# Performance work log

Hardware: AMD Instinct MI355X
Metric: run time of the kernel (lower is better)

The kernel has to match this reference:

```python
import jax, jax.numpy as jnp
import numpy as np

B, S, F, DK = 8, 2048, 1024, 128

def setup_inputs() -> dict:
    key = jax.random.key(0)
    ks = jax.random.split(key, 6)
    scale = 0.02
    return {
        "q": jax.random.normal(ks[0], (B, S, F), dtype=jnp.float32),
        "k": jax.random.normal(ks[1], (B, S, F), dtype=jnp.float32),
        "v": jax.random.normal(ks[2], (B, S, F), dtype=jnp.float32),
        "w_q": jax.random.normal(ks[3], (F, DK), dtype=jnp.float32) * scale,
        "w_k": jax.random.normal(ks[4], (F, DK), dtype=jnp.float32) * scale,
        "w_v": jax.random.normal(ks[5], (F, DK), dtype=jnp.float32) * scale,
    }

def reference(q, k, v, w_q, w_k, w_v):
    d_k = w_q.shape[-1]
    # bias-free linear projections: [B,S,F] @ [F,DK] -> [B,S,DK]
    qp = jnp.einsum("bsf,fd->bsd", q, w_q)
    kp = jnp.einsum("bsf,fd->bsd", k, w_k)
    vp = jnp.einsum("bsf,fd->bsd", v, w_v)
    # scaled dot-product scores: [B,S,S]
    scores = jnp.einsum("bqd,bkd->bqk", qp, kp) * (1.0 / jnp.sqrt(jnp.float32(d_k)))
    attn = jax.nn.softmax(scores, axis=-1)
    out = jnp.einsum("bqk,bkd->bqd", attn, vp)
    return out
```

## Files before the change

### kernel.cpp

```cpp
#include <hip/hip_runtime.h>
#include <hip/hip_bf16.h>

#define B_ 8
#define S_ 2048
#define F_ 1024
#define DK_ 128
#define M_ (B_*S_)

typedef unsigned short u16;
typedef short short8 __attribute__((ext_vector_type(8)));
typedef float f32x4 __attribute__((ext_vector_type(4)));
typedef float f32x16 __attribute__((ext_vector_type(16)));

__device__ __forceinline__ u16 f2bf(float f) {
    unsigned int u = __float_as_uint(f);
    u += 0x7FFFu + ((u >> 16) & 1u);
    return (u16)(u >> 16);
}
__device__ __forceinline__ unsigned int pack2(float a, float b) {
    return (unsigned int)f2bf(a) | ((unsigned int)f2bf(b) << 16);
}
__device__ __forceinline__ float fexp2(float x) {
#if __has_builtin(__builtin_amdgcn_exp2f)
    return __builtin_amdgcn_exp2f(x);
#else
    return exp2f(x);
#endif
}
__device__ __forceinline__ unsigned int cvt_pk_bf16(float lo, float hi) {
    unsigned int r;
    asm("v_cvt_pk_bf16_f32 %0, %1, %2" : "=v"(r) : "v"(lo), "v"(hi));
    return r;
}
__device__ __forceinline__ void pl32_swap(unsigned int& a, unsigned int& b) {
    asm("v_permlane32_swap_b32 %0, %1" : "+v"(a), "+v"(b));
}

__global__ __launch_bounds__(256) void prep_wt(const float* __restrict__ wq,
                                               const float* __restrict__ wk,
                                               const float* __restrict__ wv,
                                               u16* __restrict__ WT) {
    int id = blockIdx.x * 256 + threadIdx.x;
    if (id >= 3 * DK_ * F_) return;
    int m   = id / (DK_ * F_);
    int rem = id - m * (DK_ * F_);
    int c   = rem / F_;
    int k   = rem - c * F_;
    const float* w = (m == 0) ? wq : (m == 1) ? wk : wv;
    float v = w[k * DK_ + c];
    if (m == 0) v *= 0.12751741951f;
    WT[id] = f2bf(v);
}

__global__ __launch_bounds__(256, 3) void proj(const float* __restrict__ xq,
                                               const float* __restrict__ xk,
                                               const float* __restrict__ xv,
                                               const u16* __restrict__ WT,
                                               u16* __restrict__ qfr,
                                               u16* __restrict__ kfr,
                                               u16* __restrict__ vfr) {
    const int mode = blockIdx.y;
    const float* X = (mode == 0) ? xq : (mode == 1) ? xk : xv;
    const u16*   W = WT + mode * (DK_ * F_);

    __shared__ u16 a_lds[64][40];
    __shared__ u16 w_lds[128][40];

    const int t    = threadIdx.x;
    const int lane = t & 63;
    const int wv_  = t >> 6;
    const int l15  = lane & 15, l4 = lane >> 4;
    const int row0 = blockIdx.x * 64;

    f32x4 acc[8];
#pragma unroll
    for (int j = 0; j < 8; ++j) acc[j] = f32x4{0.f, 0.f, 0.f, 0.f};

    for (int k0 = 0; k0 < F_; k0 += 32) {
        {
            int r = t >> 2, kk = (t & 3) * 8;
            const float4* src = (const float4*)(X + (size_t)(row0 + r) * F_ + k0 + kk);
            float4 f0 = src[0], f1 = src[1];
            int4 o0;
            o0.x = pack2(f0.x, f0.y); o0.y = pack2(f0.z, f0.w);
            o0.z = pack2(f1.x, f1.y); o0.w = pack2(f1.z, f1.w);
            *(int4*)&a_lds[r][kk] = o0;
        }
        {
            int c = t >> 1, kk = (t & 1) * 16;
            const int4* src = (const int4*)(W + (size_t)c * F_ + k0 + kk);
            *(int4*)&w_lds[c][kk]     = src[0];
            *(int4*)&w_lds[c][kk + 8] = src[1];
        }
        __syncthreads();

        short8 af = *(const short8*)&a_lds[wv_ * 16 + l15][l4 * 8];
        short8 bf[8];
#pragma unroll
        for (int ct = 0; ct < 8; ++ct)
            bf[ct] = *(const short8*)&w_lds[ct * 16 + l15][l4 * 8];

        if (mode < 2) {
#pragma unroll
            for (int ct = 0; ct < 8; ++ct)
                acc[ct] = __builtin_amdgcn_mfma_f32_16x16x32_bf16(af, bf[ct], acc[ct], 0, 0, 0);
        } else {
#pragma unroll
            for (int ct = 0; ct < 8; ++ct)
                acc[ct] = __builtin_amdgcn_mfma_f32_16x16x32_bf16(bf[ct], af, acc[ct], 0, 0, 0);
        }
        __syncthreads();
    }

    if (mode < 2) {
        u16* OUT = (mode == 0) ? qfr : kfr;
#pragma unroll
        for (int ct = 0; ct < 8; ++ct)
#pragma unroll
            for (int r = 0; r < 4; ++r) {
                int q = row0 + wv_ * 16 + l4 * 4 + r;
                int d = ct * 16 + l15;
                int g = q >> 5, j = q & 31;
                int c = d >> 4, h2 = (d >> 3) & 1, e = d & 7;
                OUT[(((size_t)g * 8 + c) * 64 + h2 * 32 + j) * 8 + e] = f2bf(acc[ct][r]);
            }
    } else {
#pragma unroll
        for (int ct = 0; ct < 8; ++ct)
#pragma unroll
            for (int r = 0; r < 4; ++r) {
                int d = ct * 16 + l4 * 4 + r;
                int m = row0 + wv_ * 16 + l15;
                int g = m >> 5, ch = (m >> 4) & 1, h2 = (m >> 3) & 1, e = m & 7;
                int ct2 = d >> 5, l31 = d & 31;
                vfr[((((size_t)g * 4 + ct2) * 2 + ch) * 64 + h2 * 32 + l31) * 8 + e]
                    = f2bf(acc[ct][r]);
            }
    }
}

__global__ __launch_bounds__(512)
__attribute__((amdgpu_waves_per_eu(2)))
void attn(const u16* __restrict__ qfr,
          const u16* __restrict__ kfr,
          const u16* __restrict__ vfr,
          float* __restrict__ out) {
    __shared__ float ob[64][132];
    __shared__ float m_l[2][4][32], l_l[2][4][2][32], gm_l[2][32], gl_l[2][32];

    const int t      = threadIdx.x;
    const int lane   = t & 63;
    const int wv_    = t >> 6;
    const int q_sub  = wv_ & 1;
    const int kv_sub = wv_ >> 1;
    const int r31    = lane & 31;
    const int hi     = lane >> 5;

    const int b  = blockIdx.x & 7;
    const int qi = blockIdx.x >> 3;
    const int qrow0 = b * S_ + qi * 64;

    const size_t qg = (size_t)(b * 64 + qi * 2 + q_sub);
    short8 qf[8];
#pragma unroll
    for (int c = 0; c < 8; ++c)
        qf[c] = *(const short8*)(qfr + (qg * 8 + c) * 512 + lane * 8);

    f32x16 o4[4];
#pragma unroll
    for (int ct = 0; ct < 4; ++ct)
#pragma unroll
        for (int i = 0; i < 16; ++i) o4[ct][i] = 0.f;
    float mrun = -1.0e30f, lrun = 0.f;

    short8 kf[8];
    {
        const size_t g0 = (size_t)(b * 64 + kv_sub);
#pragma unroll
        for (int c = 0; c < 8; ++c)
            kf[c] = *(const short8*)(kfr + (g0 * 8 + c) * 512 + lane * 8);
    }

    for (int kt = 0; kt < 16; ++kt) {
        const size_t g = (size_t)(b * 64 + kt * 4 + kv_sub);

        f32x16 sa, sb;
#pragma unroll
        for (int i = 0; i < 16; ++i) { sa[i] = 0.f; sb[i] = 0.f; }
#pragma unroll
        for (int c = 0; c < 4; ++c) {
            sa = __builtin_amdgcn_mfma_f32_32x32x16_bf16(kf[c],     qf[c],     sa, 0, 0, 0);
            sb = __builtin_amdgcn_mfma_f32_32x32x16_bf16(kf[c + 4], qf[c + 4], sb, 0, 0, 0);
        }
        f32x16 st;
#pragma unroll
        for (int i = 0; i < 16; ++i) st[i] = sa[i] + sb[i];

        short8 vf[4][2];
#pragma unroll
        for (int ct = 0; ct < 4; ++ct)
#pragma unroll
            for (int ch = 0; ch < 2; ++ch)
                vf[ct][ch] = *(const short8*)(vfr + (((g * 4 + ct) * 2 + ch) * 64 + lane) * 8);

        float tm = st[0];
#pragma unroll
        for (int i = 1; i < 16; ++i) tm = fmaxf(tm, st[i]);
        if (__any(tm > mrun + 8.0f)) {
            tm = fmaxf(tm, __shfl_xor(tm, 32, 64));
            float mn = fmaxf(mrun, tm);
            float fs = fexp2(mrun - mn);
            mrun = mn;
            lrun *= fs;
#pragma unroll
            for (int ct = 0; ct < 4; ++ct)
#pragma unroll
                for (int i = 0; i < 16; ++i) o4[ct][i] *= fs;
        }
        float s0 = 0.f, s1 = 0.f;
#pragma unroll
        for (int i = 0; i < 16; i += 2) {
            st[i]     = fexp2(st[i] - mrun);
            st[i + 1] = fexp2(st[i + 1] - mrun);
            s0 += st[i]; s1 += st[i + 1];
        }
        lrun += s0 + s1;

        short8 bp[2];
#pragma unroll
        for (int ch = 0; ch < 2; ++ch) {
            unsigned int A1 = cvt_pk_bf16(st[ch * 8 + 0], st[ch * 8 + 1]);
            unsigned int A2 = cvt_pk_bf16(st[ch * 8 + 2], st[ch * 8 + 3]);
            unsigned int A3 = cvt_pk_bf16(st[ch * 8 + 4], st[ch * 8 + 5]);
            unsigned int A4 = cvt_pk_bf16(st[ch * 8 + 6], st[ch * 8 + 7]);
            pl32_swap(A1, A3);
            pl32_swap(A2, A4);
            int4 w;
            w.x = (int)A1; w.y = (int)A2; w.z = (int)A3; w.w = (int)A4;
            bp[ch] = *(short8*)&w;
        }

        if (kt < 15) {
            const size_t gn = (size_t)(b * 64 + (kt + 1) * 4 + kv_sub);
#pragma unroll
            for (int c = 0; c < 8; ++c)
                kf[c] = *(const short8*)(kfr + (gn * 8 + c) * 512 + lane * 8);
        }

#pragma unroll
        for (int ct = 0; ct < 4; ++ct) {
            o4[ct] = __builtin_amdgcn_mfma_f32_32x32x16_bf16(vf[ct][0], bp[0], o4[ct], 0, 0, 0);
            o4[ct] = __builtin_amdgcn_mfma_f32_32x32x16_bf16(vf[ct][1], bp[1], o4[ct], 0, 0, 0);
        }
    }

    __syncthreads();
    l_l[q_sub][kv_sub][hi][r31] = lrun;
    if (lane < 32) m_l[q_sub][kv_sub][r31] = mrun;
    __syncthreads();
    if (t < 64) {
        int qs = t >> 5, qq = t & 31;
        float gm = -1.0e30f;
#pragma unroll
        for (int ks = 0; ks < 4; ++ks) gm = fmaxf(gm, m_l[qs][ks][qq]);
        float gl = 0.f;
#pragma unroll
        for (int ks = 0; ks < 4; ++ks)
            gl += (l_l[qs][ks][0][qq] + l_l[qs][ks][1][qq]) * fexp2(m_l[qs][ks][qq] - gm);
        gm_l[qs][qq] = gm;
        gl_l[qs][qq] = gl;
    }
    __syncthreads();

    const float sc = fexp2(mrun - gm_l[q_sub][r31]);
    const int qrow = q_sub * 32 + r31;
    for (int rr = 0; rr < 4; ++rr) {
        if (kv_sub == rr) {
            if (rr == 0) {
#pragma unroll
                for (int ct = 0; ct < 4; ++ct)
#pragma unroll
                    for (int i = 0; i < 16; ++i) {
                        int d = ct * 32 + (i & 3) + 8 * (i >> 2) + 4 * hi;
                        ob[qrow][d] = o4[ct][i] * sc;
                    }
            } else {
#pragma unroll
                for (int ct = 0; ct < 4; ++ct)
#pragma unroll
                    for (int i = 0; i < 16; ++i) {
                        int d = ct * 32 + (i & 3) + 8 * (i >> 2) + 4 * hi;
                        ob[qrow][d] += o4[ct][i] * sc;
                    }
            }
        }
        __syncthreads();
    }

    {
        int row = t >> 3, d0 = (t & 7) * 16;
        float inv = 1.0f / gl_l[row >> 5][row & 31];
        float* dst = out + (size_t)(qrow0 + row) * DK_ + d0;
#pragma unroll
        for (int j = 0; j < 16; j += 4) {
            float4 v;
            v.x = ob[row][d0 + j]     * inv;
            v.y = ob[row][d0 + j + 1] * inv;
            v.z = ob[row][d0 + j + 2] * inv;
            v.w = ob[row][d0 + j + 3] * inv;
            *(float4*)(dst + j) = v;
        }
    }
}

extern "C" void kernel_launch(void* const* d_in, const int* in_sizes, int n_in,
                              void* d_out, int out_size, void* d_ws, size_t ws_size,
                              hipStream_t stream) {
    const float* q  = (const float*)d_in[0];
    const float* k  = (const float*)d_in[1];
    const float* v  = (const float*)d_in[2];
    const float* wq = (const float*)d_in[3];
    const float* wk = (const float*)d_in[4];
    const float* wv = (const float*)d_in[5];
    float* out = (float*)d_out;

    char* ws = (char*)d_ws;
    u16* WT  = (u16*)ws;
    u16* qfr = (u16*)(ws + 786432);
    u16* kfr = (u16*)(ws + 786432 + 4194304);
    u16* vfr = (u16*)(ws + 786432 + 2 * 4194304);

    prep_wt<<<dim3(1536), dim3(256), 0, stream>>>(wq, wk, wv, WT);
    proj<<<dim3(256, 3), dim3(256), 0, stream>>>(q, k, v, WT, qfr, kfr, vfr);
    attn<<<dim3(256), dim3(512), 0, stream>>>(qfr, kfr, vfr, out);
}
```

Before: 70.79 us.

## Double K-step to 64 and prefetch next projection tile into registers

The projection GEMM now processes 64 K-elements per iteration instead of 32, halving the number of barrier pairs. Global loads for the next tile are issued into registers before the MFMA work on the current tile and written to LDS after it, so memory latency overlaps compute. This raises register pressure (16 extra prefetch registers plus doubled fragments), which may hurt the 3-blocks-per-SM occupancy target, and LDS usage grows.

New measurement: 100.6 us. 1.42x slower.

```diff
diff --git a/kernel.cpp b/kernel.cpp
--- a/kernel.cpp
+++ b/kernel.cpp
@@ -63,8 +63,8 @@
     const float* X = (mode == 0) ? xq : (mode == 1) ? xk : xv;
     const u16*   W = WT + mode * (DK_ * F_);
 
-    __shared__ u16 a_lds[64][40];
-    __shared__ u16 w_lds[128][40];
+    __shared__ u16 a_lds[64][72];
+    __shared__ u16 w_lds[128][72];
 
     const int t    = threadIdx.x;
     const int lane = t & 63;
@@ -72,45 +72,77 @@
     const int l15  = lane & 15, l4 = lane >> 4;
     const int row0 = blockIdx.x * 64;
 
+    const int ar = t >> 2, ak = (t & 3) * 16;
+    const int wc = t >> 1, wk_ = (t & 1) * 32;
+
+    float4 ax0, ax1, ax2, ax3;
+    int4   wv0, wv1, wv2, wv3;
+
+#define LOADS(k0)                                                              \
+    {                                                                          \
+        const float4* asrc = (const float4*)(X + (size_t)(row0 + ar) * F_ + (k0) + ak); \
+        ax0 = asrc[0]; ax1 = asrc[1]; ax2 = asrc[2]; ax3 = asrc[3];            \
+        const int4* wsrc = (const int4*)(W + (size_t)wc * F_ + (k0) + wk_);    \
+        wv0 = wsrc[0]; wv1 = wsrc[1]; wv2 = wsrc[2]; wv3 = wsrc[3];            \
+    }
+#define WRITES()                                                               \
+    {                                                                          \
+        int4 o0, o1;                                                           \
+        o0.x = pack2(ax0.x, ax0.y); o0.y = pack2(ax0.z, ax0.w);                \
+        o0.z = pack2(ax1.x, ax1.y); o0.w = pack2(ax1.z, ax1.w);                \
+        o1.x = pack2(ax2.x, ax2.y); o1.y = pack2(ax2.z, ax2.w);                \
+        o1.z = pack2(ax3.x, ax3.y); o1.w = pack2(ax3.z, ax3.w);                \
+        *(int4*)&a_lds[ar][ak]      = o0;                                      \
+        *(int4*)&a_lds[ar][ak + 8]  = o1;                                      \
+        *(int4*)&w_lds[wc][wk_]      = wv0;                                    \
+        *(int4*)&w_lds[wc][wk_ + 8]  = wv1;                                    \
+        *(int4*)&w_lds[wc][wk_ + 16] = wv2;                                    \
+        *(int4*)&w_lds[wc][wk_ + 24] = wv3;                                    \
+    }
+
     f32x4 acc[8];
 #pragma unroll
     for (int j = 0; j < 8; ++j) acc[j] = f32x4{0.f, 0.f, 0.f, 0.f};
 
-    for (int k0 = 0; k0 < F_; k0 += 32) {
-        {
-            int r = t >> 2, kk = (t & 3) * 8;
-            const float4* src = (const float4*)(X + (size_t)(row0 + r) * F_ + k0 + kk);
-            float4 f0 = src[0], f1 = src[1];
-            int4 o0;
-            o0.x = pack2(f0.x, f0.y); o0.y = pack2(f0.z, f0.w);
-            o0.z = pack2(f1.x, f1.y); o0.w = pack2(f1.z, f1.w);
-            *(int4*)&a_lds[r][kk] = o0;
-        }
-        {
-            int c = t >> 1, kk = (t & 1) * 16;
-            const int4* src = (const int4*)(W + (size_t)c * F_ + k0 + kk);
-            *(int4*)&w_lds[c][kk]     = src[0];
-            *(int4*)&w_lds[c][kk + 8] = src[1];
-        }
+    LOADS(0);
+    WRITES();
+
+    for (int ks = 0; ks < 16; ++ks) {
         __syncthreads();
 
-        short8 af = *(const short8*)&a_lds[wv_ * 16 + l15][l4 * 8];
-        short8 bf[8];
+        if (ks < 15) LOADS((ks + 1) * 64);
+
+        short8 af[2], bf[8][2];
+#pragma unroll
+        for (int kc = 0; kc < 2; ++kc)
+            af[kc] = *(const short8*)&a_lds[wv_ * 16 + l15][kc * 32 + l4 * 8];
 #pragma unroll
         for (int ct = 0; ct < 8; ++ct)
-            bf[ct] = *(const short8*)&w_lds[ct * 16 + l15][l4 * 8];
+#pragma unroll
+            for (int kc = 0; kc < 2; ++kc)
+                bf[ct][kc] = *(const short8*)&w_lds[ct * 16 + l15][kc * 32 + l4 * 8];
 
         if (mode < 2) {
 #pragma unroll
-            for (int ct = 0; ct < 8; ++ct)
-                acc[ct] = __builtin_amdgcn_mfma_f32_16x16x32_bf16(af, bf[ct], acc[ct], 0, 0, 0);
+            for (int kc = 0; kc < 2; ++kc)
+#pragma unroll
+                for (int ct = 0; ct < 8; ++ct)
+                    acc[ct] = __builtin_amdgcn_mfma_f32_16x16x32_bf16(
+                        af[kc], bf[ct][kc], acc[ct], 0, 0, 0);
         } else {
 #pragma unroll
-            for (int ct = 0; ct < 8; ++ct)
-                acc[ct] = __builtin_amdgcn_mfma_f32_16x16x32_bf16(bf[ct], af, acc[ct], 0, 0, 0);
+            for (int kc = 0; kc < 2; ++kc)
+#pragma unroll
+                for (int ct = 0; ct < 8; ++ct)
+                    acc[ct] = __builtin_amdgcn_mfma_f32_16x16x32_bf16(
+                        bf[ct][kc], af[kc], acc[ct], 0, 0, 0);
         }
         __syncthreads();
-    }
+
+        if (ks < 15) WRITES();
+    }
+#undef LOADS
+#undef WRITES
 
     if (mode < 2) {
         u16* OUT = (mode == 0) ? qfr : kfr;
```
